# Performance work log

Measured on AMD Instinct MI355X. Metric: run time of the kernel, lower is better.

Reference implementation:

```python
import jax, jax.numpy as jnp
import numpy as np

N_NODES = 100000
N_EDGES = 3200000
N_GRAPHS = 32
D_IN = 128
D_HID = 128
N_CLASSES = 10


def setup_inputs() -> dict:
    key = jax.random.key(0)
    ks = jax.random.split(key, 16)
    h = jax.random.normal(ks[0], (N_NODES, D_IN), dtype=jnp.float32)
    src = jax.random.randint(ks[1], (N_EDGES,), 0, N_NODES, dtype=jnp.int32)
    dst = jax.random.randint(ks[2], (N_EDGES,), 0, N_NODES, dtype=jnp.int32)
    graph_ids = jnp.sort(jax.random.randint(ks[3], (N_NODES,), 0, N_GRAPHS, dtype=jnp.int32))
    def lin(k, fi, fo):
        s = 1.0 / np.sqrt(fi)
        kw, kb = jax.random.split(k)
        W = jax.random.uniform(kw, (fi, fo), minval=-s, maxval=s, dtype=jnp.float32)
        b = jax.random.uniform(kb, (fo,), minval=-s, maxval=s, dtype=jnp.float32)
        return W, b
    W1, b1 = lin(ks[4], D_IN, D_HID)
    W2, b2 = lin(ks[5], D_HID, D_HID)
    W3, b3 = lin(ks[6], D_HID, D_HID)
    W4, b4 = lin(ks[7], D_HID, D_HID)
    Wc1, bc1 = lin(ks[8], D_HID, D_HID)
    Wc2, bc2 = lin(ks[9], D_HID, N_CLASSES)
    return {"h": h, "src": src, "dst": dst, "graph_ids": graph_ids,
            "W1": W1, "b1": b1, "W2": W2, "b2": b2, "W3": W3, "b3": b3,
            "W4": W4, "b4": b4, "Wc1": Wc1, "bc1": bc1, "Wc2": Wc2, "bc2": bc2}


def _graph_conv(h, src, dst, inv_sqrt_out, inv_sqrt_in, W, b):
    # DGL GraphConv, norm='both': D_dst^{-1/2} A D_src^{-1/2} h W + b
    m = (h * inv_sqrt_out[:, None])[src]            # [E, D] gathered messages
    agg = jax.ops.segment_sum(m, dst, num_segments=h.shape[0])  # [N, D]
    return (agg * inv_sqrt_in[:, None]) @ W + b


def reference(h, src, dst, graph_ids, W1, b1, W2, b2, W3, b3, W4, b4, Wc1, bc1, Wc2, bc2):
    n = h.shape[0]
    ones_e = jnp.ones(src.shape[0], dtype=jnp.float32)
    out_deg = jnp.clip(jax.ops.segment_sum(ones_e, src, num_segments=n), 1.0)
    in_deg = jnp.clip(jax.ops.segment_sum(ones_e, dst, num_segments=n), 1.0)
    inv_sqrt_out = jax.lax.rsqrt(out_deg)
    inv_sqrt_in = jax.lax.rsqrt(in_deg)

    x = jax.nn.relu(_graph_conv(h, src, dst, inv_sqrt_out, inv_sqrt_in, W1, b1))
    x = jax.nn.relu(_graph_conv(x, src, dst, inv_sqrt_out, inv_sqrt_in, W2, b2))
    x = jax.nn.relu(_graph_conv(x, src, dst, inv_sqrt_out, inv_sqrt_in, W3, b3))
    x = jax.nn.relu(_graph_conv(x, src, dst, inv_sqrt_out, inv_sqrt_in, W4, b4))

    # dgl.mean_nodes over batched graphs
    sums = jax.ops.segment_sum(x, graph_ids, num_segments=N_GRAPHS)     # [G, D]
    counts = jax.ops.segment_sum(jnp.ones(n, dtype=jnp.float32), graph_ids, num_segments=N_GRAPHS)
    hg = sums / jnp.clip(counts, 1.0)[:, None]

    out = jax.nn.relu(hg @ Wc1 + bc1)
    out = out @ Wc2 + bc2
    return out
```

## Files before the change

### kernel.cpp

```cpp
#include <hip/hip_runtime.h>

#define D 128
#define NG 32
#define NC 10

typedef unsigned short ushort_t;
typedef __attribute__((ext_vector_type(8))) short short8v;
typedef __attribute__((ext_vector_type(4))) float float4v;
typedef __attribute__((ext_vector_type(2))) float float2v;

__device__ __forceinline__ ushort_t f2bf(float x) {
  union { float f; unsigned u; } v; v.f = x;
  unsigned r = (v.u + 0x7FFF + ((v.u >> 16) & 1)) >> 16;
  return (ushort_t)r;
}
__device__ __forceinline__ float bf2f(ushort_t b) {
  union { unsigned u; float f; } v; v.u = ((unsigned)b) << 16;
  return v.f;
}

__global__ void degree_kernel(const int* __restrict__ src, const int* __restrict__ dst,
                              int* __restrict__ cout_, int* __restrict__ cursor,
                              int* __restrict__ rank, int E) {
  int i = blockIdx.x * 256 + threadIdx.x;
  int e0 = i * 4;
  if (e0 + 4 <= E) {
    int4 s = *(const int4*)(src + e0);
    int4 d_ = *(const int4*)(dst + e0);
    int r0 = atomicAdd(&cursor[d_.x], 1);
    int r1 = atomicAdd(&cursor[d_.y], 1);
    int r2 = atomicAdd(&cursor[d_.z], 1);
    int r3 = atomicAdd(&cursor[d_.w], 1);
    atomicAdd(&cout_[s.x], 1);
    atomicAdd(&cout_[s.y], 1);
    atomicAdd(&cout_[s.z], 1);
    atomicAdd(&cout_[s.w], 1);
    *(int4*)(rank + e0) = make_int4(r0, r1, r2, r3);
  } else {
    for (int e = e0; e < E; ++e) {
      rank[e] = atomicAdd(&cursor[dst[e]], 1);
      atomicAdd(&cout_[src[e]], 1);
    }
  }
}

__global__ void scan1_kernel(const int* __restrict__ cnt, int* __restrict__ bsum, int n) {
  __shared__ int sdata[256];
  int base = blockIdx.x * 1024 + threadIdx.x * 4;
  int s = 0;
#pragma unroll
  for (int j = 0; j < 4; ++j) {
    int idx = base + j;
    if (idx < n) s += cnt[idx];
  }
  sdata[threadIdx.x] = s;
  __syncthreads();
  for (int off = 128; off > 0; off >>= 1) {
    if (threadIdx.x < off) sdata[threadIdx.x] += sdata[threadIdx.x + off];
    __syncthreads();
  }
  if (threadIdx.x == 0) bsum[blockIdx.x] = sdata[0];
}

__global__ void scan2_kernel(int* __restrict__ bsum, int nb) {
  __shared__ int s[1024];
  int t = threadIdx.x;
  int v = (t < nb) ? bsum[t] : 0;
  s[t] = v;
  __syncthreads();
  for (int off = 1; off < 1024; off <<= 1) {
    int add = (t >= off) ? s[t - off] : 0;
    __syncthreads();
    s[t] += add;
    __syncthreads();
  }
  if (t < nb) bsum[t] = s[t] - v;
}

__global__ void scan3_kernel(const int* __restrict__ cnt, const int* __restrict__ bsum,
                             int* __restrict__ rowptr, int n, int e_total) {
  __shared__ int ss[256];
  int t = threadIdx.x;
  int idx0 = blockIdx.x * 1024 + t * 4;
  int v[4]; int ts = 0;
#pragma unroll
  for (int j = 0; j < 4; ++j) {
    v[j] = (idx0 + j < n) ? cnt[idx0 + j] : 0;
    ts += v[j];
  }
  ss[t] = ts;
  __syncthreads();
  for (int off = 1; off < 256; off <<= 1) {
    int add = 0;
    if (t >= off) add = ss[t - off];
    __syncthreads();
    if (t >= off) ss[t] += add;
    __syncthreads();
  }
  int excl = ss[t] - ts + bsum[blockIdx.x];
#pragma unroll
  for (int j = 0; j < 4; ++j) {
    int idx = idx0 + j;
    if (idx < n) rowptr[idx] = excl;
    excl += v[j];
  }
  if (blockIdx.x == 0 && t == 0) rowptr[n] = e_total;
}

__global__ void passB_kernel(const int* __restrict__ src, const int* __restrict__ dst,
                             const int* __restrict__ rank, const int* __restrict__ rowptr,
                             int* __restrict__ csrc, int E) {
  int i = blockIdx.x * 256 + threadIdx.x;
  int e0 = i * 4;
  if (e0 + 4 <= E) {
    int4 s = *(const int4*)(src + e0);
    int4 d_ = *(const int4*)(dst + e0);
    int4 r = *(const int4*)(rank + e0);
    csrc[rowptr[d_.x] + r.x] = s.x;
    csrc[rowptr[d_.y] + r.y] = s.y;
    csrc[rowptr[d_.z] + r.z] = s.z;
    csrc[rowptr[d_.w] + r.w] = s.w;
  } else {
    for (int e = e0; e < E; ++e)
      csrc[rowptr[dst[e]] + rank[e]] = src[e];
  }
}

__global__ void cvt_h_kernel(const float* __restrict__ h, ushort_t* __restrict__ hb, long total) {
  long i4 = ((long)blockIdx.x * 256 + threadIdx.x) * 4;
  if (i4 + 4 <= total) {
    float4 v = *(const float4*)(h + i4);
    ushort_t o[4] = { f2bf(v.x), f2bf(v.y), f2bf(v.z), f2bf(v.w) };
    *(uint2*)(hb + i4) = *(const uint2*)o;
  } else {
    for (long i = i4; i < total; ++i) hb[i] = f2bf(h[i]);
  }
}

__global__ void cvt_w_kernel(const float* __restrict__ W1, const float* __restrict__ W2,
                             const float* __restrict__ W3, const float* __restrict__ W4,
                             ushort_t* __restrict__ Wt) {
  const float* Ws[4] = { W1, W2, W3, W4 };
  const float* W = Ws[blockIdx.x];
  ushort_t* o = Wt + (size_t)blockIdx.x * D * D;
  for (int idx = threadIdx.x; idx < D * D; idx += 256) {
    int c = idx >> 7, k = idx & 127;
    o[c * D + k] = f2bf(W[k * D + c]);
  }
}

__global__ __launch_bounds__(256) void gemm_mfma_kernel(const ushort_t* __restrict__ A,
    const ushort_t* __restrict__ Wt, const int* __restrict__ cout_,
    unsigned char* __restrict__ X, int n) {
  int wave = threadIdx.x >> 6;
  int lane = threadIdx.x & 63;
  int g = lane >> 4;
  int lr = lane & 15;
  int rowbase = blockIdx.x * 64 + wave * 16;
  int arow = rowbase + lr;
  int arow_c = arow < n ? arow : (n - 1);
  const ushort_t* Ap = A + (size_t)arow_c * D + g * 8;

  short8v afrag[4];
#pragma unroll
  for (int ks = 0; ks < 4; ++ks)
    afrag[ks] = *(const short8v*)(Ap + ks * 32);

  float4v acc[8];
#pragma unroll
  for (int ct = 0; ct < 8; ++ct)
#pragma unroll
    for (int r = 0; r < 4; ++r) acc[ct][r] = 0.f;

#pragma unroll
  for (int ct = 0; ct < 8; ++ct) {
    const ushort_t* bp = Wt + (size_t)(ct * 16 + lr) * D + g * 8;
#pragma unroll
    for (int ks = 0; ks < 4; ++ks) {
      short8v bfrag = *(const short8v*)(bp + ks * 32);
      acc[ct] = __builtin_amdgcn_mfma_f32_16x16x32_bf16(afrag[ks], bfrag, acc[ct], 0, 0, 0);
    }
  }

  float scv[4];
  bool rok[4];
#pragma unroll
  for (int r = 0; r < 4; ++r) {
    int grow = rowbase + g * 4 + r;
    rok[r] = grow < n;
    int gc = rok[r] ? grow : (n - 1);
    scv[r] = rsqrtf(fmaxf((float)cout_[gc], 1.f));
  }
#pragma unroll
  for (int ct = 0; ct < 8; ++ct) {
#pragma unroll
    for (int r = 0; r < 4; ++r) {
      int grow = rowbase + g * 4 + r;
      if (rok[r]) {
        int p = __builtin_amdgcn_cvt_pk_fp8_f32(acc[ct][r] * scv[r], 0.f, 0, false);
        X[(size_t)grow * D + ct * 16 + lr] = (unsigned char)(p & 0xff);
      }
    }
  }
}

#define ACC8(u)                                                                  \
  { float2v f;                                                                   \
    f = __builtin_amdgcn_cvt_pk_f32_fp8((u).x, false); acc[0] += f[0]; acc[1] += f[1]; \
    f = __builtin_amdgcn_cvt_pk_f32_fp8((u).x, true);  acc[2] += f[0]; acc[3] += f[1]; \
    f = __builtin_amdgcn_cvt_pk_f32_fp8((u).y, false); acc[4] += f[0]; acc[5] += f[1]; \
    f = __builtin_amdgcn_cvt_pk_f32_fp8((u).y, true);  acc[6] += f[0]; acc[7] += f[1]; }

__global__ __launch_bounds__(256) void agg_relu_kernel(const unsigned char* __restrict__ x,
    const int* __restrict__ rowptr, const int* __restrict__ csrc,
    const int* __restrict__ cin_, const float* __restrict__ bias,
    ushort_t* __restrict__ y, int n) {
  int node = blockIdx.x * 4 + (threadIdx.x >> 6);
  if (node >= n) return;
  int lane = threadIdx.x & 63;
  int q = lane >> 4;
  int lr = lane & 15;
  int beg = rowptr[node], end = rowptr[node + 1];
  float acc[8];
#pragma unroll
  for (int j = 0; j < 8; ++j) acc[j] = 0.f;

  const unsigned char* xp = x + lr * 8;
  int e = beg;

  int aligned = (beg + 3) & ~3;
  if (aligned > beg) {
    int ee = beg + q;
    if (ee < end && ee < aligned) {
      int s = csrc[ee];
      uint2 u = *(const uint2*)(xp + (size_t)s * D);
      ACC8(u);
    }
    e = aligned < end ? aligned : end;
  }
  for (; e + 16 <= end; e += 16) {
    int4 s4 = *(const int4*)(csrc + e + q * 4);
    uint2 u0 = *(const uint2*)(xp + (size_t)s4.x * D);
    uint2 u1 = *(const uint2*)(xp + (size_t)s4.y * D);
    uint2 u2 = *(const uint2*)(xp + (size_t)s4.z * D);
    uint2 u3 = *(const uint2*)(xp + (size_t)s4.w * D);
    ACC8(u0); ACC8(u1); ACC8(u2); ACC8(u3);
  }
  if (e + 8 <= end) {
    int s0 = csrc[e + q];
    int s1 = csrc[e + 4 + q];
    uint2 u0 = *(const uint2*)(xp + (size_t)s0 * D);
    uint2 u1 = *(const uint2*)(xp + (size_t)s1 * D);
    ACC8(u0); ACC8(u1);
    e += 8;
  }
  if (e + 4 <= end) {
    int s = csrc[e + q];
    uint2 u = *(const uint2*)(xp + (size_t)s * D);
    ACC8(u);
    e += 4;
  }
  {
    int ee = e + q;
    if (ee < end) {
      int s = csrc[ee];
      uint2 u = *(const uint2*)(xp + (size_t)s * D);
      ACC8(u);
    }
  }

#pragma unroll
  for (int j = 0; j < 8; ++j) {
    acc[j] += __shfl_xor(acc[j], 16, 64);
    acc[j] += __shfl_xor(acc[j], 32, 64);
  }
  if (q == 0) {
    float wi = rsqrtf(fmaxf((float)cin_[node], 1.f));
    float4 b0 = *(const float4*)(bias + lr * 8);
    float4 b1 = *(const float4*)(bias + lr * 8 + 4);
    ushort_t o[8];
    o[0] = f2bf(fmaxf(acc[0] * wi + b0.x, 0.f));
    o[1] = f2bf(fmaxf(acc[1] * wi + b0.y, 0.f));
    o[2] = f2bf(fmaxf(acc[2] * wi + b0.z, 0.f));
    o[3] = f2bf(fmaxf(acc[3] * wi + b0.w, 0.f));
    o[4] = f2bf(fmaxf(acc[4] * wi + b1.x, 0.f));
    o[5] = f2bf(fmaxf(acc[5] * wi + b1.y, 0.f));
    o[6] = f2bf(fmaxf(acc[6] * wi + b1.z, 0.f));
    o[7] = f2bf(fmaxf(acc[7] * wi + b1.w, 0.f));
    *(uint4*)(y + (size_t)node * D + lr * 8) = *(const uint4*)o;
  }
}

__device__ int lower_bound_gid(const int* gid, int n, int g) {
  int lo = 0, hi = n;
  while (lo < hi) { int mid = (lo + hi) >> 1; if (gid[mid] < g) lo = mid + 1; else hi = mid; }
  return lo;
}

__global__ void pool_kernel(const ushort_t* __restrict__ x, const int* __restrict__ gid,
                            float* __restrict__ sums, int* __restrict__ counts, int n) {
  int g = blockIdx.x >> 3, part = blockIdx.x & 7;
  __shared__ int s_lo, s_hi;
  if (threadIdx.x == 0) {
    s_lo = lower_bound_gid(gid, n, g);
    s_hi = lower_bound_gid(gid, n, g + 1);
    if (part == 0) counts[g] = s_hi - s_lo;
  }
  __syncthreads();
  int lo = s_lo, hi = s_hi;
  int cnt = hi - lo;
  int per = (cnt + 7) >> 3;
  int a = lo + part * per;
  int bnd = min(a + per, hi);
  int t = threadIdx.x;
  float acc = 0.f;
  for (int i = a; i < bnd; ++i) acc += bf2f(x[(size_t)i * D + t]);
  atomicAdd(&sums[g * D + t], acc);
}

__global__ __launch_bounds__(128) void classifier_kernel(const float* __restrict__ sums,
    const int* __restrict__ counts, const float* __restrict__ Wc1, const float* __restrict__ bc1,
    const float* __restrict__ Wc2, const float* __restrict__ bc2, float* __restrict__ out) {
  __shared__ float hg[NG][D];
  __shared__ float hid[NG][D];
  int t = threadIdx.x;
#pragma unroll
  for (int g = 0; g < NG; ++g)
    hg[g][t] = sums[g * D + t] / fmaxf((float)counts[g], 1.f);
  __syncthreads();
  float acc[NG];
#pragma unroll
  for (int g = 0; g < NG; ++g) acc[g] = bc1[t];
  for (int k = 0; k < D; ++k) {
    float w = Wc1[k * D + t];
#pragma unroll
    for (int g = 0; g < NG; ++g) acc[g] += hg[g][k] * w;
  }
#pragma unroll
  for (int g = 0; g < NG; ++g) hid[g][t] = fmaxf(acc[g], 0.f);
  __syncthreads();
  for (int idx = t; idx < NG * NC; idx += 128) {
    int g = idx / NC, c = idx % NC;
    float a = bc2[c];
    for (int j = 0; j < D; ++j) a += hid[g][j] * Wc2[j * NC + c];
    out[idx] = a;
  }
}

extern "C" void kernel_launch(void* const* d_in, const int* in_sizes, int n_in,
                              void* d_out, int out_size, void* d_ws, size_t ws_size,
                              hipStream_t stream) {
  const float* h   = (const float*)d_in[0];
  const int* src   = (const int*)d_in[1];
  const int* dst   = (const int*)d_in[2];
  const int* gid   = (const int*)d_in[3];
  const float* W1  = (const float*)d_in[4];
  const float* b1  = (const float*)d_in[5];
  const float* W2  = (const float*)d_in[6];
  const float* b2  = (const float*)d_in[7];
  const float* W3  = (const float*)d_in[8];
  const float* b3  = (const float*)d_in[9];
  const float* W4  = (const float*)d_in[10];
  const float* b4  = (const float*)d_in[11];
  const float* Wc1 = (const float*)d_in[12];
  const float* bc1 = (const float*)d_in[13];
  const float* Wc2 = (const float*)d_in[14];
  const float* bc2 = (const float*)d_in[15];
  float* out = (float*)d_out;

  const int N = in_sizes[3];
  const int E = in_sizes[1];

  char* ws = (char*)d_ws;
  size_t off = 0;
  auto alloc = [&](size_t bytes) -> char* {
    char* p = ws + off;
    off = (off + bytes + 255) & ~(size_t)255;
    return p;
  };

  int* cnts     = (int*)alloc((size_t)2 * N * 4);
  int* cout_    = cnts;
  int* cursor   = cnts + N;
  int* rowptr   = (int*)alloc((size_t)(N + 1) * 4);
  int* bsum     = (int*)alloc(4096);
  int* csrc     = (int*)alloc((size_t)E * 4);
  ushort_t* Wt  = (ushort_t*)alloc((size_t)4 * D * D * 2);
  unsigned char* Xb = (unsigned char*)alloc((size_t)N * D);
  ushort_t* Yb  = (ushort_t*)alloc((size_t)N * D * 2);
  float* sums   = (float*)alloc((size_t)(NG * D + NG) * 4);
  int* counts   = (int*)(sums + NG * D);
  int* rank     = (int*)Yb;
  ushort_t* Hb  = Yb;

  hipMemsetAsync(cnts, 0, (size_t)2 * N * 4, stream);
  hipMemsetAsync(sums, 0, (size_t)(NG * D + NG) * 4, stream);

  int gE4 = (E / 4 + 255) / 256 + 1;
  int nb  = (N + 1023) / 1024;
  int gAgg  = (N + 3) / 4;
  int gGemm = (N + 63) / 64;
  long totalH = (long)N * D;
  int gCvt = (int)((totalH / 4 + 255) / 256) + 1;

  degree_kernel<<<gE4, 256, 0, stream>>>(src, dst, cout_, cursor, rank, E);
  scan1_kernel<<<nb, 256, 0, stream>>>(cursor, bsum, N);
  scan2_kernel<<<1, 1024, 0, stream>>>(bsum, nb);
  scan3_kernel<<<nb, 256, 0, stream>>>(cursor, bsum, rowptr, N, E);
  passB_kernel<<<gE4, 256, 0, stream>>>(src, dst, rank, rowptr, csrc, E);

  cvt_w_kernel<<<4, 256, 0, stream>>>(W1, W2, W3, W4, Wt);
  cvt_h_kernel<<<gCvt, 256, 0, stream>>>(h, Hb, totalH);

  gemm_mfma_kernel<<<gGemm, 256, 0, stream>>>(Hb, Wt, cout_, Xb, N);
  agg_relu_kernel<<<gAgg, 256, 0, stream>>>(Xb, rowptr, csrc, cursor, b1, Yb, N);
  gemm_mfma_kernel<<<gGemm, 256, 0, stream>>>(Yb, Wt + (size_t)1 * D * D, cout_, Xb, N);
  agg_relu_kernel<<<gAgg, 256, 0, stream>>>(Xb, rowptr, csrc, cursor, b2, Yb, N);
  gemm_mfma_kernel<<<gGemm, 256, 0, stream>>>(Yb, Wt + (size_t)2 * D * D, cout_, Xb, N);
  agg_relu_kernel<<<gAgg, 256, 0, stream>>>(Xb, rowptr, csrc, cursor, b3, Yb, N);
  gemm_mfma_kernel<<<gGemm, 256, 0, stream>>>(Yb, Wt + (size_t)3 * D * D, cout_, Xb, N);
  agg_relu_kernel<<<gAgg, 256, 0, stream>>>(Xb, rowptr, csrc, cursor, b4, Yb, N);

  pool_kernel<<<NG * 8, 128, 0, stream>>>(Yb, gid, sums, counts, N);
  classifier_kernel<<<1, 128, 0, stream>>>(sums, counts, Wc1, bc1, Wc2, bc2, out);
}
```

Measured before the change: 914.8 us.

## Fuse aggregation+ReLU with next layer GEMM via LDS tile

Adds a kernel that aggregates 64 nodes per block (16 per wave, sequentially), applies normalization, bias and ReLU, stores the bf16 rows in shared memory, then runs the next layer's MFMA GEMM and writes fp8 output. This removes the intermediate bf16 Y round trip and three separate launches for layers 2-4. Buffers are re-aliased so the fp8 ping-pong buffers do not overlap. The risk is lower parallelism: each wave now handles 16 nodes serially instead of one node per wave, which can hurt latency hiding in the gather-bound aggregation.

```diff
diff --git a/kernel.cpp b/kernel.cpp
--- a/kernel.cpp
+++ b/kernel.cpp
@@ -211,6 +211,138 @@
     f = __builtin_amdgcn_cvt_pk_f32_fp8((u).y, false); acc[4] += f[0]; acc[5] += f[1]; \
     f = __builtin_amdgcn_cvt_pk_f32_fp8((u).y, true);  acc[6] += f[0]; acc[7] += f[1]; }
 
+__global__ __launch_bounds__(256) void fused_agg_gemm_kernel(
+    const unsigned char* __restrict__ x, const int* __restrict__ rowptr,
+    const int* __restrict__ csrc, const int* __restrict__ cin_,
+    const float* __restrict__ bias, const ushort_t* __restrict__ Wt,
+    const int* __restrict__ cout_, unsigned char* __restrict__ Xout, int n) {
+  __shared__ ushort_t As[64][136];
+  int wave = threadIdx.x >> 6;
+  int lane = threadIdx.x & 63;
+  int q = lane >> 4;
+  int lr = lane & 15;
+  int nodebase = blockIdx.x * 64 + wave * 16;
+  const unsigned char* xp = x + lr * 8;
+
+  for (int i = 0; i < 16; ++i) {
+    int node = nodebase + i;
+    float acc[8];
+#pragma unroll
+    for (int j = 0; j < 8; ++j) acc[j] = 0.f;
+    if (node < n) {
+      int beg = rowptr[node], end = rowptr[node + 1];
+      int e = beg;
+      int pro = (beg + 3) & ~3;
+      if (pro > beg) {
+        int ee = beg + q;
+        if (ee < end && ee < pro) {
+          int s = csrc[ee];
+          uint2 u = *(const uint2*)(xp + (size_t)s * D);
+          ACC8(u);
+        }
+        e = pro < end ? pro : end;
+      }
+      for (; e + 16 <= end; e += 16) {
+        int4 s4 = *(const int4*)(csrc + e + q * 4);
+        uint2 u0 = *(const uint2*)(xp + (size_t)s4.x * D);
+        uint2 u1 = *(const uint2*)(xp + (size_t)s4.y * D);
+        uint2 u2 = *(const uint2*)(xp + (size_t)s4.z * D);
+        uint2 u3 = *(const uint2*)(xp + (size_t)s4.w * D);
+        ACC8(u0); ACC8(u1); ACC8(u2); ACC8(u3);
+      }
+      if (e + 8 <= end) {
+        int s0 = csrc[e + q];
+        int s1 = csrc[e + 4 + q];
+        uint2 u0 = *(const uint2*)(xp + (size_t)s0 * D);
+        uint2 u1 = *(const uint2*)(xp + (size_t)s1 * D);
+        ACC8(u0); ACC8(u1);
+        e += 8;
+      }
+      if (e + 4 <= end) {
+        int s = csrc[e + q];
+        uint2 u = *(const uint2*)(xp + (size_t)s * D);
+        ACC8(u);
+        e += 4;
+      }
+      {
+        int ee = e + q;
+        if (ee < end) {
+          int s = csrc[ee];
+          uint2 u = *(const uint2*)(xp + (size_t)s * D);
+          ACC8(u);
+        }
+      }
+#pragma unroll
+      for (int j = 0; j < 8; ++j) {
+        acc[j] += __shfl_xor(acc[j], 16, 64);
+        acc[j] += __shfl_xor(acc[j], 32, 64);
+      }
+      if (q == 0) {
+        float wi = rsqrtf(fmaxf((float)cin_[node], 1.f));
+        float4 b0 = *(const float4*)(bias + lr * 8);
+        float4 b1 = *(const float4*)(bias + lr * 8 + 4);
+        ushort_t o[8];
+        o[0] = f2bf(fmaxf(acc[0] * wi + b0.x, 0.f));
+        o[1] = f2bf(fmaxf(acc[1] * wi + b0.y, 0.f));
+        o[2] = f2bf(fmaxf(acc[2] * wi + b0.z, 0.f));
+        o[3] = f2bf(fmaxf(acc[3] * wi + b0.w, 0.f));
+        o[4] = f2bf(fmaxf(acc[4] * wi + b1.x, 0.f));
+        o[5] = f2bf(fmaxf(acc[5] * wi + b1.y, 0.f));
+        o[6] = f2bf(fmaxf(acc[6] * wi + b1.z, 0.f));
+        o[7] = f2bf(fmaxf(acc[7] * wi + b1.w, 0.f));
+        *(uint4*)&As[wave * 16 + i][lr * 8] = *(const uint4*)o;
+      }
+    } else if (q == 0) {
+      ushort_t z[8] = {0, 0, 0, 0, 0, 0, 0, 0};
+      *(uint4*)&As[wave * 16 + i][lr * 8] = *(const uint4*)z;
+    }
+  }
+  __syncthreads();
+
+  int arow_l = wave * 16 + lr;
+  short8v afrag[4];
+#pragma unroll
+  for (int ks = 0; ks < 4; ++ks)
+    afrag[ks] = *(const short8v*)&As[arow_l][q * 8 + ks * 32];
+
+  float4v accv[8];
+#pragma unroll
+  for (int ct = 0; ct < 8; ++ct)
+#pragma unroll
+    for (int r = 0; r < 4; ++r) accv[ct][r] = 0.f;
+
+#pragma unroll
+  for (int ct = 0; ct < 8; ++ct) {
+    const ushort_t* bp = Wt + (size_t)(ct * 16 + lr) * D + q * 8;
+#pragma unroll
+    for (int ks = 0; ks < 4; ++ks) {
+      short8v bfrag = *(const short8v*)(bp + ks * 32);
+      accv[ct] = __builtin_amdgcn_mfma_f32_16x16x32_bf16(afrag[ks], bfrag, accv[ct], 0, 0, 0);
+    }
+  }
+
+  float scv[4];
+  bool rok[4];
+#pragma unroll
+  for (int r = 0; r < 4; ++r) {
+    int grow = nodebase + q * 4 + r;
+    rok[r] = grow < n;
+    int gc = rok[r] ? grow : (n - 1);
+    scv[r] = rsqrtf(fmaxf((float)cout_[gc], 1.f));
+  }
+#pragma unroll
+  for (int ct = 0; ct < 8; ++ct) {
+#pragma unroll
+    for (int r = 0; r < 4; ++r) {
+      int grow = nodebase + q * 4 + r;
+      if (rok[r]) {
+        int p = __builtin_amdgcn_cvt_pk_fp8_f32(accv[ct][r] * scv[r], 0.f, 0, false);
+        Xout[(size_t)grow * D + ct * 16 + lr] = (unsigned char)(p & 0xff);
+      }
+    }
+  }
+}
+
 __global__ __launch_bounds__(256) void agg_relu_kernel(const unsigned char* __restrict__ x,
     const int* __restrict__ rowptr, const int* __restrict__ csrc,
     const int* __restrict__ cin_, const float* __restrict__ bias,
@@ -227,16 +359,15 @@
 
   const unsigned char* xp = x + lr * 8;
   int e = beg;
-
-  int aligned = (beg + 3) & ~3;
-  if (aligned > beg) {
+  int pro = (beg + 3) & ~3;
+  if (pro > beg) {
     int ee = beg + q;
-    if (ee < end && ee < aligned) {
+    if (ee < end && ee < pro) {
       int s = csrc[ee];
       uint2 u = *(const uint2*)(xp + (size_t)s * D);
       ACC8(u);
     }
-    e = aligned < end ? aligned : end;
+    e = pro < end ? pro : end;
   }
   for (; e + 16 <= end; e += 16) {
     int4 s4 = *(const int4*)(csrc + e + q * 4);
@@ -386,12 +517,14 @@
   int* bsum     = (int*)alloc(4096);
   int* csrc     = (int*)alloc((size_t)E * 4);
   ushort_t* Wt  = (ushort_t*)alloc((size_t)4 * D * D * 2);
-  unsigned char* Xb = (unsigned char*)alloc((size_t)N * D);
+  unsigned char* Xb = (unsigned char*)alloc((size_t)N * D * 2);
   ushort_t* Yb  = (ushort_t*)alloc((size_t)N * D * 2);
   float* sums   = (float*)alloc((size_t)(NG * D + NG) * 4);
   int* counts   = (int*)(sums + NG * D);
   int* rank     = (int*)Yb;
   ushort_t* Hb  = Yb;
+  unsigned char* Xa8 = (unsigned char*)Yb;
+  ushort_t* Y4  = (ushort_t*)Xb;
 
   hipMemsetAsync(cnts, 0, (size_t)2 * N * 4, stream);
   hipMemsetAsync(sums, 0, (size_t)(NG * D + NG) * 4, stream);
@@ -399,7 +532,7 @@
   int gE4 = (E / 4 + 255) / 256 + 1;
   int nb  = (N + 1023) / 1024;
   int gAgg  = (N + 3) / 4;
-  int gGemm = (N + 63) / 64;
+  int gF    = (N + 63) / 64;
   long totalH = (long)N * D;
   int gCvt = (int)((totalH / 4 + 255) / 256) + 1;
 
@@ -412,15 +545,15 @@
   cvt_w_kernel<<<4, 256, 0, stream>>>(W1, W2, W3, W4, Wt);
   cvt_h_kernel<<<gCvt, 256, 0, stream>>>(h, Hb, totalH);
 
-  gemm_mfma_kernel<<<gGemm, 256, 0, stream>>>(Hb, Wt, cout_, Xb, N);
-  agg_relu_kernel<<<gAgg, 256, 0, stream>>>(Xb, rowptr, csrc, cursor, b1, Yb, N);
-  gemm_mfma_kernel<<<gGemm, 256, 0, stream>>>(Yb, Wt + (size_t)1 * D * D, cout_, Xb, N);
-  agg_relu_kernel<<<gAgg, 256, 0, stream>>>(Xb, rowptr, csrc, cursor, b2, Yb, N);
-  gemm_mfma_kernel<<<gGemm, 256, 0, stream>>>(Yb, Wt + (size_t)2 * D * D, cout_, Xb, N);
-  agg_relu_kernel<<<gAgg, 256, 0, stream>>>(Xb, rowptr, csrc, cursor, b3, Yb, N);
-  gemm_mfma_kernel<<<gGemm, 256, 0, stream>>>(Yb, Wt + (size_t)3 * D * D, cout_, Xb, N);
-  agg_relu_kernel<<<gAgg, 256, 0, stream>>>(Xb, rowptr, csrc, cursor, b4, Yb, N);
-
-  pool_kernel<<<NG * 8, 128, 0, stream>>>(Yb, gid, sums, counts, N);
+  gemm_mfma_kernel<<<gF, 256, 0, stream>>>(Hb, Wt, cout_, Xb, N);
+  fused_agg_gemm_kernel<<<gF, 256, 0, stream>>>(Xb, rowptr, csrc, cursor, b1,
+                                                Wt + (size_t)1 * D * D, cout_, Xa8, N);
+  fused_agg_gemm_kernel<<<gF, 256, 0, stream>>>(Xa8, rowptr, csrc, cursor, b2,
+                                                Wt + (size_t)2 * D * D, cout_, Xb, N);
+  fused_agg_gemm_kernel<<<gF, 256, 0, stream>>>(Xb, rowptr, csrc, cursor, b3,
+                                                Wt + (size_t)3 * D * D, cout_, Xa8, N);
+  agg_relu_kernel<<<gAgg, 256, 0, stream>>>(Xa8, rowptr, csrc, cursor, b4, Y4, N);
+
+  pool_kernel<<<NG * 8, 128, 0, stream>>>(Y4, gid, sums, counts, N);
   classifier_kernel<<<1, 128, 0, stream>>>(sums, counts, Wc1, bc1, Wc2, bc2, out);
 }
```

Result: slower. 1.040 ms (+13.7%).
